# Kernel optimization log

Measured on AMD Instinct MI355X. Metric: run time of the kernel, lower is better.

The kernel has to match this reference:

```python
import jax, jax.numpy as jnp
import numpy as np
from jax import lax

EPS_RADIUS = 1e-3  # eps_radius from __init__


def setup_inputs() -> dict:
    key = jax.random.key(0)
    ks = jax.random.split(key, 8)
    Bsz, L, H, N, O = 16, 4096, 512, 512, 512
    n_pairs = N // 2
    return {
        "input": jax.random.normal(ks[0], (Bsz, L, H), dtype=jnp.float32),
        "state": jnp.zeros((Bsz, N), dtype=jnp.float32),
        "S": 0.1 * jax.random.normal(ks[1], (N, N), dtype=jnp.float32),
        "rho_raw": 0.01 * jax.random.normal(ks[2], (n_pairs,), dtype=jnp.float32),
        "theta": 0.01 * jax.random.normal(ks[3], (n_pairs,), dtype=jnp.float32),
        "K12_raw": 0.5 * jax.random.normal(ks[4], (N, H), dtype=jnp.float32),
        "K21_raw": 0.5 * jax.random.normal(ks[5], (O, N), dtype=jnp.float32),
        "K22_raw": 0.5 * jax.random.normal(ks[6], (O, H), dtype=jnp.float32),
        "log_gamma": jnp.zeros((), dtype=jnp.float32),  # gamma = 1.0
    }


def _dense_ssm_matrices(S, rho_raw, theta, K12_raw, K21_raw, K22_raw, log_gamma):
    N = S.shape[0]
    n_pairs = N // 2
    # K11 structured: block-diag 2x2 rotation-scaling blocks
    rho = jax.nn.sigmoid(rho_raw) * (1.0 - EPS_RADIUS)
    c, s = jnp.cos(theta), jnp.sin(theta)
    ii = jnp.arange(n_pairs) * 2
    K11 = jnp.zeros((N, N), dtype=S.dtype)
    K11 = (K11.at[ii, ii].set(rho * c)
               .at[ii, ii + 1].set(-rho * s)
               .at[ii + 1, ii].set(rho * s)
               .at[ii + 1, ii + 1].set(rho * c))
    # assemble full K and spectrally normalize (exact norm via SVD)
    K_raw = jnp.block([[K11, K12_raw], [K21_raw, K22_raw]])
    sigma = jnp.maximum(jnp.linalg.norm(K_raw, ord=2), 1e-5)
    K = K_raw / (sigma + 0.002)
    K11n = K[:N, :N]
    K12n = K[:N, N:]
    K21n = K[N:, :N]
    K22n = K[N:, N:]
    gamma = jnp.exp(log_gamma)
    Sinv = jnp.linalg.inv(S)
    A = Sinv @ K11n @ S          # (N, N)
    B = gamma * (Sinv @ K12n)    # (N, H)
    C = K21n @ S                 # (O, N)
    D = gamma * K22n             # (O, H)
    return A, B, C, D


def reference(input, state, S, rho_raw, theta, K12_raw, K21_raw, K22_raw, log_gamma):
    A, B, C, D = _dense_ssm_matrices(S, rho_raw, theta, K12_raw, K21_raw, K22_raw, log_gamma)
    u = input  # (Bsz, L, H)
    Bu = jnp.einsum('blh,nh->lbn', u, B)  # precompute input projections, (L, Bsz, N)

    def step(x, bu_t):
        x_new = x @ A.T + bu_t  # (Bsz, N)
        return x_new, x_new

    _, xs = lax.scan(step, state, Bu)  # xs: (L, Bsz, N), states x_1..x_L
    # y_t = C x_t + D u_t uses pre-states x_0..x_{L-1}
    pre = jnp.concatenate([state[None], xs[:-1]], axis=0)  # (L, Bsz, N)
    y = jnp.einsum('lbn,on->blo', pre, C) + jnp.einsum('blh,oh->blo', u, D)
    return y
```

## Files before the change

### kernel.cpp

```cpp
#include <hip/hip_runtime.h>
#include <stdint.h>


#define LM 40
#define CHUNK 128
#define WARM 12
#define LBLK 32

typedef float f32x4 __attribute__((ext_vector_type(4)));
typedef __bf16 bf16x8 __attribute__((ext_vector_type(8)));
typedef unsigned int u32;
typedef unsigned long long u64;
typedef unsigned short u16;

static __device__ __forceinline__ u16 f2bf(float f){
  u32 u = __float_as_uint(f);
  u32 r = (u + 0x7fffu + ((u >> 16) & 1u)) >> 16;
  return (u16)r;
}

static __device__ __forceinline__ float kraw_at(int i, int j,
    const float* rho_raw, const float* theta,
    const float* K12, const float* K21, const float* K22){
  if (i < 512){
    if (j < 512){
      if ((i >> 1) != (j >> 1)) return 0.f;
      int p = i >> 1;
      float rho = (1.f / (1.f + expf(-rho_raw[p]))) * 0.999f;
      float c = cosf(theta[p]), s = sinf(theta[p]);
      return ((i & 1) == 0) ? (((j & 1) == 0) ? rho * c : -rho * s)
                            : (((j & 1) == 0) ? rho * s :  rho * c);
    }
    return K12[i * 512 + (j - 512)];
  }
  if (j < 512) return K21[(i - 512) * 512 + j];
  return K22[(i - 512) * 512 + (j - 512)];
}

static __device__ __forceinline__ void gload16(const u16* g, u16* l){
  __builtin_amdgcn_global_load_lds((const __attribute__((address_space(1))) u32*)g,
                                   (__attribute__((address_space(3))) u32*)l, 16, 0, 0);
}

template <typename OT>
static __device__ __forceinline__ void gemm_body(int g, int ngrid,
    const u16* __restrict__ A, int lda, const u16* __restrict__ B, int ldb,
    OT* __restrict__ C, int ldc, int K, int ntn){
  __shared__ u16 As[128 * 64];
  __shared__ u16 Bs[128 * 64];
  int xcd = g & 7, local = g >> 3;
  int mper = (ngrid >> 3) / ntn;
  int bn = local % ntn;
  int bm = xcd * mper + local / ntn;
  int t = threadIdx.x, lane = t & 63, wave = t >> 6;
  int lrow = t >> 3;
  int swz = (((t & 7) ^ (lrow & 7)) << 3);
  const u16* Ag = A + (size_t)(bm * 128 + lrow) * lda + swz;
  const u16* Bg = B + (size_t)(bn * 128 + lrow) * ldb + swz;
  u16* Asd = As + t * 8;
  u16* Bsd = Bs + t * 8;
  f32x4 acc[4][4];
  #pragma unroll
  for (int mi = 0; mi < 4; ++mi)
    #pragma unroll
    for (int ni = 0; ni < 4; ++ni) acc[mi][ni] = (f32x4){0.f, 0.f, 0.f, 0.f};
  int wm = (wave & 1) << 6, wn = (wave >> 1) << 6;
  int fr = lane & 15, cbb = lane >> 4;
  for (int kt = 0; kt < K; kt += 64){
    __syncthreads();
    #pragma unroll
    for (int r = 0; r < 4; ++r){
      gload16(Ag + (size_t)(r * 32) * lda + kt, Asd + r * 2048);
      gload16(Bg + (size_t)(r * 32) * ldb + kt, Bsd + r * 2048);
    }
    __syncthreads();
    #pragma unroll
    for (int kk = 0; kk < 2; ++kk){
      bf16x8 af[4], bfr[4];
      #pragma unroll
      for (int mi = 0; mi < 4; ++mi){
        int row = wm + mi * 16 + fr;
        int pcb = ((kk << 2) + cbb) ^ (fr & 7);
        af[mi] = *(const bf16x8*)(As + row * 64 + pcb * 8);
      }
      #pragma unroll
      for (int ni = 0; ni < 4; ++ni){
        int row = wn + ni * 16 + fr;
        int pcb = ((kk << 2) + cbb) ^ (fr & 7);
        bfr[ni] = *(const bf16x8*)(Bs + row * 64 + pcb * 8);
      }
      #pragma unroll
      for (int mi = 0; mi < 4; ++mi)
        #pragma unroll
        for (int ni = 0; ni < 4; ++ni)
          acc[mi][ni] = __builtin_amdgcn_mfma_f32_16x16x32_bf16(af[mi], bfr[ni], acc[mi][ni], 0, 0, 0);
    }
  }
  int rq = lane >> 4;
  #pragma unroll
  for (int mi = 0; mi < 4; ++mi)
    #pragma unroll
    for (int ni = 0; ni < 4; ++ni){
      size_t base = (size_t)(bm * 128 + wm + mi * 16 + rq * 4) * ldc
                  + (size_t)(bn * 128 + wn + ni * 16 + fr);
      #pragma unroll
      for (int r = 0; r < 4; ++r){
        if constexpr (sizeof(OT) == 4) C[base + (size_t)r * ldc] = acc[mi][ni][r];
        else                           C[base + (size_t)r * ldc] = (OT)f2bf(acc[mi][ni][r]);
      }
    }
}

__global__ __launch_bounds__(256) void kA(const float* rho_raw, const float* theta,
    const float* K12, const float* K21, const float* K22, u16* KTbf,
    const float4* k12_4, u16* W12, u64* rec){
  int blk = blockIdx.x;
  if (blk < 4096){
    int idx = blk * 256 + threadIdx.x;
    int j = idx >> 10, i = idx & 1023;
    KTbf[idx] = f2bf(kraw_at(i, j, rho_raw, theta, K12, K21, K22));
  } else if (blk < 4096 + 256){
    long g = (long)(blk - 4096) * 256 + threadIdx.x;
    float4 v = k12_4[g];
    u32 lo = (u32)f2bf(v.x) | ((u32)f2bf(v.y) << 16);
    u32 hi = (u32)f2bf(v.z) | ((u32)f2bf(v.w) << 16);
    ((uint2*)W12)[g] = make_uint2(lo, hi);
  } else {
    for (int i = threadIdx.x; i < 2048; i += 256) rec[i] = 0ull;
  }
}

__global__ __launch_bounds__(256) void kB(const u16* KTbf, float* G,
    const float4* u4, u16* X, const float* S, const float* state, float* w0){
  int blk = blockIdx.x;
  if (blk < 64){
    gemm_body<float>(blk, 64, KTbf, 1024, KTbf, 1024, G, 1024, 1024, 8);
  } else if (blk < 64 + 32768){
    long g = (long)(blk - 64) * 256 + threadIdx.x;
    float4 v = u4[g];
    int h4 = (int)(g & 127);
    long row = g >> 7;
    u16* dst = X + row * 1024 + 512 + h4 * 4;
    u32 lo = (u32)f2bf(v.x) | ((u32)f2bf(v.y) << 16);
    u32 hi = (u32)f2bf(v.z) | ((u32)f2bf(v.w) << 16);
    *((uint2*)dst) = make_uint2(lo, hi);
  } else {
    int idx = (blk - 32832) * 256 + threadIdx.x;
    int b = idx >> 9, n = idx & 511;
    const float* sr = S + n * 512;
    const float* st = state + b * 512;
    float acc = 0.f;
    for (int m2 = 0; m2 < 512; ++m2) acc += sr[m2] * st[m2];
    w0[idx] = acc;
  }
}

__global__ __launch_bounds__(256, 1) void kC(const float* __restrict__ G,
    u64* rec, const float* rho_raw, const float* theta, const float* log_gamma,
    float* scal, float2* coef,
    const u16* Xb, const u16* W12, u16* Bu){
  if (blockIdx.x >= LBLK){
    gemm_body<u16>(blockIdx.x - LBLK, 2048, Xb, 1024, W12, 512, Bu, 512, 512, 4);
    return;
  }
  __shared__ __align__(16) float vl[1024];
  __shared__ float red[8];
  __shared__ double sa[LM], sb2[LM + 1];
  __shared__ float sh_inv;
  int t = threadIdx.x, wave = t >> 6, lane = t & 63;
  int row0 = blockIdx.x * 32;

  f32x4 greg[8][4];
  {
    const float* gbase = G + (size_t)(row0 + wave * 8) * 1024 + lane * 4;
    #pragma unroll
    for (int rr = 0; rr < 8; ++rr)
      #pragma unroll
      for (int i2 = 0; i2 < 4; ++i2)
        greg[rr][i2] = *(const f32x4*)(gbase + (size_t)rr * 1024 + i2 * 256);
  }

  float vprevreg[4] = {0.f, 0.f, 0.f, 0.f};
  float n2tot;
  {
    float s = 0.f;
    #pragma unroll
    for (int k = 0; k < 4; ++k){
      int i = t + 256 * k;
      float v = sinf(0.613f * (float)i + 0.271f) + 0.3f * sinf(0.0247f * (float)i + 1.3f);
      vl[i] = v;
      s += v * v;
    }
    #pragma unroll
    for (int off = 32; off; off >>= 1) s += __shfl_down(s, off);
    if (lane == 0) red[wave] = s;
    __syncthreads();
    n2tot = (red[0] + red[1]) + (red[2] + red[3]);
  }
  float scl = 1.f / sqrtf(n2tot);
  float betacoef = 0.f;
  if (t == 0) sb2[0] = 0.0;

  for (int j = 1; j <= LM; ++j){
    u64* rb = rec + ((j & 1) ? 0 : 1024);
    {
      f32x4 vreg[4];
      #pragma unroll
      for (int i2 = 0; i2 < 4; ++i2)
        vreg[i2] = *((const f32x4*)vl + lane + 64 * i2);
      u64 myrec = 0ull;
      #pragma unroll
      for (int rr = 0; rr < 8; ++rr){
        float s = 0.f;
        #pragma unroll
        for (int i2 = 0; i2 < 4; ++i2){
          f32x4 g = greg[rr][i2], v = vreg[i2];
          s += g[0] * v[0] + g[1] * v[1] + g[2] * v[2] + g[3] * v[3];
        }
        #pragma unroll
        for (int off = 32; off; off >>= 1) s += __shfl_xor(s, off);
        if (lane == rr)
          myrec = ((u64)(u32)j << 32) | (u64)__float_as_uint(s);
      }
      if (lane < 8)
        __hip_atomic_store(&rb[row0 + wave * 8 + lane], myrec,
                           __ATOMIC_RELAXED, __HIP_MEMORY_SCOPE_AGENT);
    }

    float yr[4], vr[4];
    {
      u64 r0, r1, r2, r3;
      bool done = false;
      while (!done){
        r0 = __hip_atomic_load(&rb[t        ], __ATOMIC_RELAXED, __HIP_MEMORY_SCOPE_AGENT);
        r1 = __hip_atomic_load(&rb[t +  256 ], __ATOMIC_RELAXED, __HIP_MEMORY_SCOPE_AGENT);
        r2 = __hip_atomic_load(&rb[t +  512 ], __ATOMIC_RELAXED, __HIP_MEMORY_SCOPE_AGENT);
        r3 = __hip_atomic_load(&rb[t +  768 ], __ATOMIC_RELAXED, __HIP_MEMORY_SCOPE_AGENT);
        done = ((u32)(r0 >> 32) == (u32)j) && ((u32)(r1 >> 32) == (u32)j)
            && ((u32)(r2 >> 32) == (u32)j) && ((u32)(r3 >> 32) == (u32)j);
        if (!done) __builtin_amdgcn_s_sleep(1);
      }
      yr[0] = __uint_as_float((u32)r0); yr[1] = __uint_as_float((u32)r1);
      yr[2] = __uint_as_float((u32)r2); yr[3] = __uint_as_float((u32)r3);
      #pragma unroll
      for (int k = 0; k < 4; ++k) vr[k] = vl[t + 256 * k];
    }

    float dotp = 0.f;
    #pragma unroll
    for (int k = 0; k < 4; ++k) dotp += vr[k] * yr[k];
    #pragma unroll
    for (int off = 32; off; off >>= 1) dotp += __shfl_down(dotp, off);
    if (lane == 0) red[wave] = dotp;
    __syncthreads();
    float dot = (red[0] + red[1]) + (red[2] + red[3]);
    float alpha_f = dot * scl * scl;

    float n2 = 0.f;
    #pragma unroll
    for (int k = 0; k < 4; ++k){
      float vh = vr[k] * scl;
      float wv = yr[k] * scl - alpha_f * vh - betacoef * vprevreg[k];
      vprevreg[k] = vh;
      vl[t + 256 * k] = wv;
      n2 += wv * wv;
    }
    #pragma unroll
    for (int off = 32; off; off >>= 1) n2 += __shfl_down(n2, off);
    if (lane == 0) red[4 + wave] = n2;
    __syncthreads();
    n2tot = (red[4] + red[5]) + (red[6] + red[7]);
    if (n2tot < 1e-30f) n2tot = 1e-30f;

    if (t == 0){ sa[j - 1] = (double)alpha_f; sb2[j] = (double)n2tot; }
    betacoef = sqrtf(n2tot);
    scl = 1.f / betacoef;
  }

  if (blockIdx.x != 0) return;
  __syncthreads();
  if (t < 64){
    int lane2 = t;
    double lo = sa[0], hi = sa[0], bmax = 0.0;
    for (int i = 0; i < LM; ++i){
      if (sa[i] > lo) lo = sa[i];
      double bl = (i > 0) ? sqrt(fmax(sb2[i], 0.0)) : 0.0;
      double br = (i < LM - 1) ? sqrt(fmax(sb2[i + 1], 0.0)) : 0.0;
      double g = sa[i] + bl + br;
      if (g > hi) hi = g;
      if (i < LM - 1 && sb2[i + 1] > bmax) bmax = sb2[i + 1];
    }
    hi = hi + 1e-6 * fabs(hi) + 1e-20;
    lo = lo - 1e-6 * fabs(lo) - 1e-20;
    double pivmin = 1e-30 * bmax + 1e-300;
    for (int round = 0; round < 6; ++round){
      double x = lo + (hi - lo) * ((double)(lane2 + 1) / 65.0);
      double d = sa[0] - x; int cnt = (d < 0.0);
      for (int i = 1; i < LM; ++i){
        if (fabs(d) < pivmin) d = -pivmin;
        d = (sa[i] - x) - sb2[i] / d;
        cnt += (d < 0.0);
      }
      unsigned long long mk = __ballot(cnt >= LM);
      int bpos = (mk == 0ULL) ? 64 : (__ffsll((unsigned long long)mk) - 1);
      double xlo = __shfl(x, (bpos == 0) ? 0 : bpos - 1);
      double xhi = __shfl(x, (bpos == 64) ? 63 : bpos);
      double nlo = (bpos == 0) ? lo : xlo;
      double nhi = (bpos == 64) ? hi : xhi;
      lo = nlo; hi = nhi;
    }
    if (lane2 == 0){
      double lam = 0.5 * (lo + hi);
      double sig = (lam > 0.0) ? sqrt(lam) : 0.0;
      if (sig < 1e-5) sig = 1e-5;
      double spp = sig + 0.002;
      float inv = (float)(1.0 / spp);
      float g = expf(log_gamma[0]);
      scal[0] = inv; scal[1] = g; scal[2] = g * inv;
      sh_inv = inv;
    }
  }
  __syncthreads();
  float inv = sh_inv;
  float rho = (1.f / (1.f + expf(-rho_raw[t]))) * 0.999f;
  float c = cosf(theta[t]), s = sinf(theta[t]);
  coef[t] = make_float2(rho * c * inv, rho * s * inv);
}

__global__ __launch_bounds__(256) void kD(const u32* Bu, const float2* coef,
    const float* w0, const float* scal, u16* X,
    const float* K21, const float* K22, u16* W){
  int blk = blockIdx.x;
  if (blk >= 512){
    int idx = (blk - 512) * 256 + threadIdx.x;
    int o = idx >> 10, c = idx & 1023;
    float inv = scal[0], gi = scal[2];
    float v = (c < 512) ? K21[o * 512 + c] * inv : K22[o * 512 + (c - 512)] * gi;
    W[idx] = f2bf(v);
    return;
  }
  int b = blk >> 5;
  int c = blk & 31;
  int p = threadIdx.x;
  float2 ab = coef[p];
  float gi = scal[2];
  int t0 = c * CHUNK;
  float wx, wy; int t;
  if (c == 0){ wx = w0[b * 512 + 2 * p]; wy = w0[b * 512 + 2 * p + 1]; t = 0; }
  else { wx = 0.f; wy = 0.f; t = t0 - WARM; }
  const u32* bub = Bu + (size_t)b * 4096 * 256;
  u16* xb = X + (size_t)b * 4096 * 1024;
  for (; t < t0; ++t){
    u32 v = bub[(size_t)t * 256 + p];
    float bx = __uint_as_float(v << 16);
    float by = __uint_as_float(v & 0xffff0000u);
    float nx = ab.x * wx - ab.y * wy + gi * bx;
    float ny = ab.y * wx + ab.x * wy + gi * by;
    wx = nx; wy = ny;
  }
  for (; t < t0 + CHUNK; ++t){
    u32 pk = (u32)f2bf(wx) | ((u32)f2bf(wy) << 16);
    *(u32*)(xb + (size_t)t * 1024 + 2 * p) = pk;
    u32 v = bub[(size_t)t * 256 + p];
    float bx = __uint_as_float(v << 16);
    float by = __uint_as_float(v & 0xffff0000u);
    float nx = ab.x * wx - ab.y * wy + gi * bx;
    float ny = ab.y * wx + ab.x * wy + gi * by;
    wx = nx; wy = ny;
  }
}

template <typename OT>
__global__ __launch_bounds__(256) void gemm_nt(const u16* __restrict__ A, int lda,
    const u16* __restrict__ B, int ldb, OT* __restrict__ C, int ldc, int K, int ntn){
  gemm_body<OT>(blockIdx.x, gridDim.x, A, lda, B, ldb, C, ldc, K, ntn);
}

extern "C" void kernel_launch(void* const* d_in, const int* in_sizes, int n_in,
                              void* d_out, int out_size, void* d_ws, size_t ws_size,
                              hipStream_t stream){
  const float* u        = (const float*)d_in[0];
  const float* state    = (const float*)d_in[1];
  const float* S        = (const float*)d_in[2];
  const float* rho_raw  = (const float*)d_in[3];
  const float* theta    = (const float*)d_in[4];
  const float* K12      = (const float*)d_in[5];
  const float* K21      = (const float*)d_in[6];
  const float* K22      = (const float*)d_in[7];
  const float* log_gamma= (const float*)d_in[8];

  char* w = (char*)d_ws;
  size_t off = 0;
  auto alloc = [&](size_t bytes)->void*{
    void* p = w + off;
    off = (off + bytes + 255) & ~(size_t)255;
    return p;
  };
  u64*    rec   = (u64*)alloc(2048 * 8);
  float*  scal  = (float*)alloc(64);
  float2* coef  = (float2*)alloc(256 * 8);
  float*  w0    = (float*)alloc(16 * 512 * 4);
  u16*    KTbf  = (u16*)alloc((size_t)1024 * 1024 * 2);
  float*  G     = (float*)alloc((size_t)1024 * 1024 * 4);
  u16*    W12   = (u16*)alloc((size_t)512 * 512 * 2);
  u16*    Wcat  = (u16*)alloc((size_t)512 * 1024 * 2);
  u16*    Xb    = (u16*)alloc((size_t)65536 * 1024 * 2);
  u16*    Bu    = (u16*)d_out;

  kA<<<4353, 256, 0, stream>>>(rho_raw, theta, K12, K21, K22, KTbf,
                               (const float4*)K12, W12, rec);
  kB<<<32864, 256, 0, stream>>>(KTbf, G, (const float4*)u, Xb, S, state, w0);
  kC<<<LBLK + 2048, 256, 0, stream>>>(G, rec, rho_raw, theta, log_gamma,
                                      scal, coef, Xb + 512, W12, Bu);
  kD<<<2560, 256, 0, stream>>>((const u32*)Bu, coef, w0, scal, Xb, K21, K22, Wcat);
  gemm_nt<float><<<2048, 256, 0, stream>>>(Xb, 1024, Wcat, 1024, (float*)d_out, 512, 1024, 4);
}
```

Before: 552.1 us.

## Split output GEMM: compute u·K22 alongside Bu GEMM, fold in final pass

The D·u term of the output is computed unscaled in kC, as extra GEMM blocks that run in the same launch as the Bu projection, and written to the output buffer. The final GEMM then covers only the K21 (state) half, with K=512 instead of 1024, and adds the scaled stored partial in its epilogue. Bu moves into a separate workspace buffer when it fits. This moves half of the final GEMM off the critical path after the serial scan. The cost is an extra read-modify-write of the fp32 output and more workspace.

```diff
diff --git a/kernel.cpp b/kernel.cpp
--- a/kernel.cpp
+++ b/kernel.cpp
@@ -42,10 +42,10 @@
                                    (__attribute__((address_space(3))) u32*)l, 16, 0, 0);
 }
 
-template <typename OT>
+template <typename OT, int MODE>
 static __device__ __forceinline__ void gemm_body(int g, int ngrid,
     const u16* __restrict__ A, int lda, const u16* __restrict__ B, int ldb,
-    OT* __restrict__ C, int ldc, int K, int ntn){
+    OT* __restrict__ C, int ldc, int K, int ntn, const float* accs){
   __shared__ u16 As[128 * 64];
   __shared__ u16 Bs[128 * 64];
   int xcd = g & 7, local = g >> 3;
@@ -96,6 +96,8 @@
           acc[mi][ni] = __builtin_amdgcn_mfma_f32_16x16x32_bf16(af[mi], bfr[ni], acc[mi][ni], 0, 0, 0);
     }
   }
+  float s = 0.f;
+  if constexpr (MODE == 1) s = accs[2];
   int rq = lane >> 4;
   #pragma unroll
   for (int mi = 0; mi < 4; ++mi)
@@ -105,15 +107,22 @@
                   + (size_t)(bn * 128 + wn + ni * 16 + fr);
       #pragma unroll
       for (int r = 0; r < 4; ++r){
-        if constexpr (sizeof(OT) == 4) C[base + (size_t)r * ldc] = acc[mi][ni][r];
-        else                           C[base + (size_t)r * ldc] = (OT)f2bf(acc[mi][ni][r]);
+        size_t idx = base + (size_t)r * ldc;
+        if constexpr (MODE == 1){
+          float old = C[idx];
+          C[idx] = acc[mi][ni][r] + s * old;
+        } else if constexpr (sizeof(OT) == 4){
+          C[idx] = acc[mi][ni][r];
+        } else {
+          C[idx] = (OT)f2bf(acc[mi][ni][r]);
+        }
       }
     }
 }
 
 __global__ __launch_bounds__(256) void kA(const float* rho_raw, const float* theta,
     const float* K12, const float* K21, const float* K22, u16* KTbf,
-    const float4* k12_4, u16* W12, u64* rec){
+    const float4* k12_4, u16* W12, const float4* k22_4, u16* K22bf, u64* rec){
   int blk = blockIdx.x;
   if (blk < 4096){
     int idx = blk * 256 + threadIdx.x;
@@ -125,6 +134,12 @@
     u32 lo = (u32)f2bf(v.x) | ((u32)f2bf(v.y) << 16);
     u32 hi = (u32)f2bf(v.z) | ((u32)f2bf(v.w) << 16);
     ((uint2*)W12)[g] = make_uint2(lo, hi);
+  } else if (blk < 4096 + 512){
+    long g = (long)(blk - 4352) * 256 + threadIdx.x;
+    float4 v = k22_4[g];
+    u32 lo = (u32)f2bf(v.x) | ((u32)f2bf(v.y) << 16);
+    u32 hi = (u32)f2bf(v.z) | ((u32)f2bf(v.w) << 16);
+    ((uint2*)K22bf)[g] = make_uint2(lo, hi);
   } else {
     for (int i = threadIdx.x; i < 2048; i += 256) rec[i] = 0ull;
   }
@@ -134,7 +149,7 @@
     const float4* u4, u16* X, const float* S, const float* state, float* w0){
   int blk = blockIdx.x;
   if (blk < 64){
-    gemm_body<float>(blk, 64, KTbf, 1024, KTbf, 1024, G, 1024, 1024, 8);
+    gemm_body<float, 0>(blk, 64, KTbf, 1024, KTbf, 1024, G, 1024, 1024, 8, nullptr);
   } else if (blk < 64 + 32768){
     long g = (long)(blk - 64) * 256 + threadIdx.x;
     float4 v = u4[g];
@@ -158,9 +173,15 @@
 __global__ __launch_bounds__(256, 1) void kC(const float* __restrict__ G,
     u64* rec, const float* rho_raw, const float* theta, const float* log_gamma,
     float* scal, float2* coef,
-    const u16* Xb, const u16* W12, u16* Bu){
+    const u16* Xu, const u16* W12, u16* Bu, const u16* K22bf, float* Y2){
+  if (blockIdx.x >= LBLK + 2048){
+    gemm_body<float, 0>(blockIdx.x - LBLK - 2048, 2048, Xu, 1024, K22bf, 512,
+                        Y2, 512, 512, 4, nullptr);
+    return;
+  }
   if (blockIdx.x >= LBLK){
-    gemm_body<u16>(blockIdx.x - LBLK, 2048, Xb, 1024, W12, 512, Bu, 512, 512, 4);
+    gemm_body<u16, 0>(blockIdx.x - LBLK, 2048, Xu, 1024, W12, 512, Bu, 512,
+                      512, 4, nullptr);
     return;
   }
   __shared__ __align__(16) float vl[1024];
@@ -329,14 +350,19 @@
 
 __global__ __launch_bounds__(256) void kD(const u32* Bu, const float2* coef,
     const float* w0, const float* scal, u16* X,
-    const float* K21, const float* K22, u16* W){
+    const float* K21, const float* K22, u16* W, int wcols){
   int blk = blockIdx.x;
   if (blk >= 512){
     int idx = (blk - 512) * 256 + threadIdx.x;
-    int o = idx >> 10, c = idx & 1023;
-    float inv = scal[0], gi = scal[2];
-    float v = (c < 512) ? K21[o * 512 + c] * inv : K22[o * 512 + (c - 512)] * gi;
-    W[idx] = f2bf(v);
+    float inv = scal[0], gi2 = scal[2];
+    if (wcols == 1024){
+      int o = idx >> 10, c = idx & 1023;
+      float v = (c < 512) ? K21[o * 512 + c] * inv : K22[o * 512 + (c - 512)] * gi2;
+      W[idx] = f2bf(v);
+    } else {
+      int o = idx >> 9, c = idx & 511;
+      W[idx] = f2bf(K21[o * 512 + c] * inv);
+    }
     return;
   }
   int b = blk >> 5;
@@ -370,10 +396,11 @@
   }
 }
 
-template <typename OT>
+template <typename OT, int MODE>
 __global__ __launch_bounds__(256) void gemm_nt(const u16* __restrict__ A, int lda,
-    const u16* __restrict__ B, int ldb, OT* __restrict__ C, int ldc, int K, int ntn){
-  gemm_body<OT>(blockIdx.x, gridDim.x, A, lda, B, ldb, C, ldc, K, ntn);
+    const u16* __restrict__ B, int ldb, OT* __restrict__ C, int ldc, int K,
+    int ntn, const float* accs){
+  gemm_body<OT, MODE>(blockIdx.x, gridDim.x, A, lda, B, ldb, C, ldc, K, ntn, accs);
 }
 
 extern "C" void kernel_launch(void* const* d_in, const int* in_sizes, int n_in,
@@ -403,15 +430,27 @@
   u16*    KTbf  = (u16*)alloc((size_t)1024 * 1024 * 2);
   float*  G     = (float*)alloc((size_t)1024 * 1024 * 4);
   u16*    W12   = (u16*)alloc((size_t)512 * 512 * 2);
+  u16*    K22bf = (u16*)alloc((size_t)512 * 512 * 2);
   u16*    Wcat  = (u16*)alloc((size_t)512 * 1024 * 2);
   u16*    Xb    = (u16*)alloc((size_t)65536 * 1024 * 2);
-  u16*    Bu    = (u16*)d_out;
-
-  kA<<<4353, 256, 0, stream>>>(rho_raw, theta, K12, K21, K22, KTbf,
-                               (const float4*)K12, W12, rec);
+  u16*    BuWs  = (u16*)alloc((size_t)65536 * 512 * 2);
+  bool split = (off <= ws_size);
+  u16*    Bu    = split ? BuWs : (u16*)d_out;
+
+  kA<<<4609, 256, 0, stream>>>(rho_raw, theta, K12, K21, K22, KTbf,
+                               (const float4*)K12, W12,
+                               (const float4*)K22, K22bf, rec);
   kB<<<32864, 256, 0, stream>>>(KTbf, G, (const float4*)u, Xb, S, state, w0);
-  kC<<<LBLK + 2048, 256, 0, stream>>>(G, rec, rho_raw, theta, log_gamma,
-                                      scal, coef, Xb + 512, W12, Bu);
-  kD<<<2560, 256, 0, stream>>>((const u32*)Bu, coef, w0, scal, Xb, K21, K22, Wcat);
-  gemm_nt<float><<<2048, 256, 0, stream>>>(Xb, 1024, Wcat, 1024, (float*)d_out, 512, 1024, 4);
-}
+  kC<<<LBLK + 2048 + (split ? 2048 : 0), 256, 0, stream>>>(
+      G, rec, rho_raw, theta, log_gamma, scal, coef,
+      Xb + 512, W12, Bu, K22bf, (float*)d_out);
+  kD<<<512 + (split ? 1024 : 2048), 256, 0, stream>>>(
+      (const u32*)Bu, coef, w0, scal, Xb, K21, K22, Wcat, split ? 512 : 1024);
+  if (split){
+    gemm_nt<float, 1><<<2048, 256, 0, stream>>>(Xb, 1024, Wcat, 512,
+                                                (float*)d_out, 512, 512, 4, scal);
+  } else {
+    gemm_nt<float, 0><<<2048, 256, 0, stream>>>(Xb, 1024, Wcat, 1024,
+                                                (float*)d_out, 512, 1024, 4, nullptr);
+  }
+}
```

New measurement: 643.5 us. 1.17x slower.

## Merge input-conversion into kA and move Gram GEMM into kC with flag sync

Applied to the files above, without the earlier changes.

The kB kernel is removed. Its input bf16 conversion and w0 work move into kA, and the K^T K Gram GEMM moves into kC as 64 extra blocks. Those blocks write G with agent-scope atomic stores and bump a global counter, and the Lanczos blocks spin on that counter before reading G. This saves one launch and lets the Bu GEMM blocks run alongside the Gram GEMM, at the cost of a spin-wait that relies on the 64 GEMM blocks being scheduled before or alongside the waiting blocks.

```diff
diff --git a/kernel.cpp b/kernel.cpp
--- a/kernel.cpp
+++ b/kernel.cpp
@@ -42,12 +42,10 @@
                                    (__attribute__((address_space(3))) u32*)l, 16, 0, 0);
 }
 
-template <typename OT>
+template <typename OT, int MODE>
 static __device__ __forceinline__ void gemm_body(int g, int ngrid,
     const u16* __restrict__ A, int lda, const u16* __restrict__ B, int ldb,
-    OT* __restrict__ C, int ldc, int K, int ntn){
-  __shared__ u16 As[128 * 64];
-  __shared__ u16 Bs[128 * 64];
+    OT* __restrict__ C, int ldc, int K, int ntn, u16* As, u16* Bs){
   int xcd = g & 7, local = g >> 3;
   int mper = (ngrid >> 3) / ntn;
   int bn = local % ntn;
@@ -105,38 +103,40 @@
                   + (size_t)(bn * 128 + wn + ni * 16 + fr);
       #pragma unroll
       for (int r = 0; r < 4; ++r){
-        if constexpr (sizeof(OT) == 4) C[base + (size_t)r * ldc] = acc[mi][ni][r];
-        else                           C[base + (size_t)r * ldc] = (OT)f2bf(acc[mi][ni][r]);
+        size_t idx = base + (size_t)r * ldc;
+        if constexpr (MODE == 2){
+          __hip_atomic_store((float*)&C[idx], acc[mi][ni][r],
+                             __ATOMIC_RELAXED, __HIP_MEMORY_SCOPE_AGENT);
+        } else if constexpr (sizeof(OT) == 4){
+          C[idx] = acc[mi][ni][r];
+        } else {
+          C[idx] = (OT)f2bf(acc[mi][ni][r]);
+        }
       }
     }
 }
 
 __global__ __launch_bounds__(256) void kA(const float* rho_raw, const float* theta,
     const float* K12, const float* K21, const float* K22, u16* KTbf,
-    const float4* k12_4, u16* W12, u64* rec){
+    const float4* k12_4, u16* W12, u64* rec, u32* gflag,
+    const float4* u4, u16* X, const float* S, const float* state, float* w0){
   int blk = blockIdx.x;
+  int t = threadIdx.x;
   if (blk < 4096){
-    int idx = blk * 256 + threadIdx.x;
+    int idx = blk * 256 + t;
     int j = idx >> 10, i = idx & 1023;
     KTbf[idx] = f2bf(kraw_at(i, j, rho_raw, theta, K12, K21, K22));
-  } else if (blk < 4096 + 256){
-    long g = (long)(blk - 4096) * 256 + threadIdx.x;
+  } else if (blk < 4352){
+    long g = (long)(blk - 4096) * 256 + t;
     float4 v = k12_4[g];
     u32 lo = (u32)f2bf(v.x) | ((u32)f2bf(v.y) << 16);
     u32 hi = (u32)f2bf(v.z) | ((u32)f2bf(v.w) << 16);
     ((uint2*)W12)[g] = make_uint2(lo, hi);
-  } else {
-    for (int i = threadIdx.x; i < 2048; i += 256) rec[i] = 0ull;
-  }
-}
-
-__global__ __launch_bounds__(256) void kB(const u16* KTbf, float* G,
-    const float4* u4, u16* X, const float* S, const float* state, float* w0){
-  int blk = blockIdx.x;
-  if (blk < 64){
-    gemm_body<float>(blk, 64, KTbf, 1024, KTbf, 1024, G, 1024, 1024, 8);
-  } else if (blk < 64 + 32768){
-    long g = (long)(blk - 64) * 256 + threadIdx.x;
+  } else if (blk == 4352){
+    for (int i = t; i < 2048; i += 256) rec[i] = 0ull;
+    if (t == 0) gflag[0] = 0u;
+  } else if (blk < 4353 + 32768){
+    long g = (long)(blk - 4353) * 256 + t;
     float4 v = u4[g];
     int h4 = (int)(g & 127);
     long row = g >> 7;
@@ -145,7 +145,7 @@
     u32 hi = (u32)f2bf(v.z) | ((u32)f2bf(v.w) << 16);
     *((uint2*)dst) = make_uint2(lo, hi);
   } else {
-    int idx = (blk - 32832) * 256 + threadIdx.x;
+    int idx = (blk - 37121) * 256 + t;
     int b = idx >> 9, n = idx & 511;
     const float* sr = S + n * 512;
     const float* st = state + b * 512;
@@ -155,12 +155,26 @@
   }
 }
 
-__global__ __launch_bounds__(256, 1) void kC(const float* __restrict__ G,
-    u64* rec, const float* rho_raw, const float* theta, const float* log_gamma,
+__global__ __launch_bounds__(256, 1) void kC(const u16* __restrict__ KTbf,
+    float* G, u32* gflag, u64* rec,
+    const float* rho_raw, const float* theta, const float* log_gamma,
     float* scal, float2* coef,
-    const u16* Xb, const u16* W12, u16* Bu){
-  if (blockIdx.x >= LBLK){
-    gemm_body<u16>(blockIdx.x - LBLK, 2048, Xb, 1024, W12, 512, Bu, 512, 512, 4);
+    const u16* Xu, const u16* W12, u16* Bu){
+  __shared__ __align__(16) u16 smA[128 * 64];
+  __shared__ __align__(16) u16 smB[128 * 64];
+  int blk = blockIdx.x;
+  if (blk < 64){
+    gemm_body<float, 2>(blk, 64, KTbf, 1024, KTbf, 1024, G, 1024, 1024, 8,
+                        smA, smB);
+    asm volatile("s_waitcnt vmcnt(0)" ::: "memory");
+    __syncthreads();
+    if (threadIdx.x == 0)
+      __hip_atomic_fetch_add(gflag, 1u, __ATOMIC_RELAXED, __HIP_MEMORY_SCOPE_AGENT);
+    return;
+  }
+  if (blk >= 64 + LBLK){
+    gemm_body<u16, 0>(blk - 64 - LBLK, 2048, Xu, 1024, W12, 512, Bu, 512,
+                      512, 4, smA, smB);
     return;
   }
   __shared__ __align__(16) float vl[1024];
@@ -168,7 +182,13 @@
   __shared__ double sa[LM], sb2[LM + 1];
   __shared__ float sh_inv;
   int t = threadIdx.x, wave = t >> 6, lane = t & 63;
-  int row0 = blockIdx.x * 32;
+  int row0 = (blk - 64) * 32;
+
+  if (t == 0){
+    while (__hip_atomic_load(gflag, __ATOMIC_RELAXED, __HIP_MEMORY_SCOPE_AGENT) < 64u)
+      __builtin_amdgcn_s_sleep(2);
+  }
+  __syncthreads();
 
   f32x4 greg[8][4];
   {
@@ -277,7 +297,7 @@
     scl = 1.f / betacoef;
   }
 
-  if (blockIdx.x != 0) return;
+  if (blk != 64) return;
   __syncthreads();
   if (t < 64){
     int lane2 = t;
@@ -334,8 +354,8 @@
   if (blk >= 512){
     int idx = (blk - 512) * 256 + threadIdx.x;
     int o = idx >> 10, c = idx & 1023;
-    float inv = scal[0], gi = scal[2];
-    float v = (c < 512) ? K21[o * 512 + c] * inv : K22[o * 512 + (c - 512)] * gi;
+    float inv = scal[0], gi2 = scal[2];
+    float v = (c < 512) ? K21[o * 512 + c] * inv : K22[o * 512 + (c - 512)] * gi2;
     W[idx] = f2bf(v);
     return;
   }
@@ -370,10 +390,13 @@
   }
 }
 
-template <typename OT>
+template <typename OT, int MODE>
 __global__ __launch_bounds__(256) void gemm_nt(const u16* __restrict__ A, int lda,
     const u16* __restrict__ B, int ldb, OT* __restrict__ C, int ldc, int K, int ntn){
-  gemm_body<OT>(blockIdx.x, gridDim.x, A, lda, B, ldb, C, ldc, K, ntn);
+  __shared__ __align__(16) u16 smA[128 * 64];
+  __shared__ __align__(16) u16 smB[128 * 64];
+  gemm_body<OT, MODE>(blockIdx.x, gridDim.x, A, lda, B, ldb, C, ldc, K, ntn,
+                      smA, smB);
 }
 
 extern "C" void kernel_launch(void* const* d_in, const int* in_sizes, int n_in,
@@ -397,6 +420,7 @@
     return p;
   };
   u64*    rec   = (u64*)alloc(2048 * 8);
+  u32*    gflag = (u32*)alloc(256);
   float*  scal  = (float*)alloc(64);
   float2* coef  = (float2*)alloc(256 * 8);
   float*  w0    = (float*)alloc(16 * 512 * 4);
@@ -407,11 +431,13 @@
   u16*    Xb    = (u16*)alloc((size_t)65536 * 1024 * 2);
   u16*    Bu    = (u16*)d_out;
 
-  kA<<<4353, 256, 0, stream>>>(rho_raw, theta, K12, K21, K22, KTbf,
-                               (const float4*)K12, W12, rec);
-  kB<<<32864, 256, 0, stream>>>(KTbf, G, (const float4*)u, Xb, S, state, w0);
-  kC<<<LBLK + 2048, 256, 0, stream>>>(G, rec, rho_raw, theta, log_gamma,
-                                      scal, coef, Xb + 512, W12, Bu);
+  kA<<<37153, 256, 0, stream>>>(rho_raw, theta, K12, K21, K22, KTbf,
+                                (const float4*)K12, W12, rec, gflag,
+                                (const float4*)u, Xb, S, state, w0);
+  kC<<<64 + LBLK + 2048, 256, 0, stream>>>(KTbf, G, gflag, rec,
+                                           rho_raw, theta, log_gamma,
+                                           scal, coef, Xb + 512, W12, Bu);
   kD<<<2560, 256, 0, stream>>>((const u32*)Bu, coef, w0, scal, Xb, K21, K22, Wcat);
-  gemm_nt<float><<<2048, 256, 0, stream>>>(Xb, 1024, Wcat, 1024, (float*)d_out, 512, 1024, 4);
-}
+  gemm_nt<float, 0><<<2048, 256, 0, stream>>>(Xb, 1024, Wcat, 1024,
+                                              (float*)d_out, 512, 1024, 4);
+}
```

New measurement: 557.6 us. No clear change (+1.0%).
